# Kernel optimization log

Hardware: AMD Instinct MI355X
Metric: run time of the kernel (lower is better)

Reference implementation:

```python
import jax, jax.numpy as jnp
import numpy as np

DIM = 512
H = 8
HD = DIM // H
B = 1
S = 4096
SCALE = HD ** -0.5


def setup_inputs() -> dict:
    key = jax.random.key(0)
    k1, k2, k3, k4, k5 = jax.random.split(key, 5)
    bound = DIM ** -0.5
    x = jax.random.normal(k1, (B, S, DIM), dtype=jnp.float32)
    q_param = jax.random.uniform(k2, (DIM, H, HD), dtype=jnp.float32, minval=-bound, maxval=bound)
    k_param = jax.random.uniform(k3, (DIM, H, HD), dtype=jnp.float32, minval=-bound, maxval=bound)
    v_param = jax.random.uniform(k4, (DIM, H, HD), dtype=jnp.float32, minval=-bound, maxval=bound)
    p_param = jax.random.uniform(k5, (H, HD, DIM), dtype=jnp.float32, minval=-bound, maxval=bound)
    return {"x": x, "q_param": q_param, "k_param": k_param, "v_param": v_param, "p_param": p_param}


def reference(x, q_param, k_param, v_param, p_param):
    q = jnp.einsum('bsc,chd->bshd', x, q_param) * SCALE
    k = jnp.einsum('btc,chd->bthd', x, k_param)
    v = jnp.einsum('btc,chd->bthd', x, v_param)
    attn = jax.nn.softmax(jnp.einsum('bshd,bthd->bhst', q, k), axis=-1)  # [B,H,S,S]
    o = jnp.einsum('bhst,bthd->bshd', attn, v)
    return jnp.einsum('bshd,hdc->bsc', o, p_param)
```

## Files before the change

### kernel.cpp

```cpp
#include <hip/hip_runtime.h>
#include <hip/hip_bf16.h>
#include <stdint.h>

#define S_LEN 4096
#define DIM   512
#define NH    8
#define HD    64
#define QSCALE 0.18033688011112042f

typedef __attribute__((ext_vector_type(8))) short short8;
typedef __attribute__((ext_vector_type(4))) float f32x4;
typedef __attribute__((ext_vector_type(16))) float f32x16;
typedef __attribute__((ext_vector_type(2))) unsigned uint2v;

__device__ __forceinline__ uint32_t pk2(float lo, float hi) {
  union { __hip_bfloat162 h; uint32_t u; } cv;
  cv.h = __float22bfloat162_rn(float2{lo, hi});
  return cv.u;
}
__device__ __forceinline__ ushort bf1(float x) {
  union { __hip_bfloat16 b; ushort u; } cv;
  cv.b = __float2bfloat16(x);
  return cv.u;
}
__device__ __forceinline__ float bf2f(ushort u) {
  union { uint32_t u; float f; } cv;
  cv.u = (uint32_t)u << 16;
  return cv.f;
}

__global__ __launch_bounds__(256)
void cast_x(const float* __restrict__ src, ushort* __restrict__ dst) {
  const int i = (blockIdx.x * 256 + threadIdx.x) * 8;
  const float4 a = *reinterpret_cast<const float4*>(src + i);
  const float4 b = *reinterpret_cast<const float4*>(src + i + 4);
  uint4 o;
  o.x = pk2(a.x, a.y); o.y = pk2(a.z, a.w);
  o.z = pk2(b.x, b.y); o.w = pk2(b.z, b.w);
  *reinterpret_cast<uint4*>(dst + i) = o;
}

__global__ __launch_bounds__(256)
void transpose_w(const float* __restrict__ qp, const float* __restrict__ kp,
                 const float* __restrict__ vp, const float* __restrict__ pp,
                 ushort* __restrict__ wbT, ushort* __restrict__ ppT) {
  __shared__ float L[64][65];
  const int z = blockIdx.z;
  const float* src = (z == 0) ? qp : (z == 1) ? kp : (z == 2) ? vp : pp;
  ushort* dst = (z < 3) ? (wbT + (size_t)z * 512 * 512) : ppT;
  const float scale = (z == 0) ? QSCALE : 1.0f;
  const int k0 = blockIdx.x * 64, n0 = blockIdx.y * 64;
  const int r = threadIdx.x >> 2, c0 = (threadIdx.x & 3) * 16;

#pragma unroll
  for (int j = 0; j < 4; ++j) {
    const float4 v =
        *reinterpret_cast<const float4*>(&src[(k0 + r) * 512 + n0 + c0 + 4 * j]);
    L[r][c0 + 4 * j + 0] = v.x * scale;
    L[r][c0 + 4 * j + 1] = v.y * scale;
    L[r][c0 + 4 * j + 2] = v.z * scale;
    L[r][c0 + 4 * j + 3] = v.w * scale;
  }
  __syncthreads();

  uint4 u0, u1;
  u0.x = pk2(L[c0 + 0][r], L[c0 + 1][r]);
  u0.y = pk2(L[c0 + 2][r], L[c0 + 3][r]);
  u0.z = pk2(L[c0 + 4][r], L[c0 + 5][r]);
  u0.w = pk2(L[c0 + 6][r], L[c0 + 7][r]);
  u1.x = pk2(L[c0 + 8][r], L[c0 + 9][r]);
  u1.y = pk2(L[c0 + 10][r], L[c0 + 11][r]);
  u1.z = pk2(L[c0 + 12][r], L[c0 + 13][r]);
  u1.w = pk2(L[c0 + 14][r], L[c0 + 15][r]);
  ushort* d = dst + (size_t)(n0 + r) * 512 + k0 + c0;
  *reinterpret_cast<uint4*>(d) = u0;
  *reinterpret_cast<uint4*>(d + 8) = u1;
}

template <int MODE>
__global__ __launch_bounds__(256)
void gemm_bf16(const ushort* __restrict__ A, const ushort* __restrict__ Bt,
               void* __restrict__ Cout) {
  __shared__ __align__(16) unsigned char lds[24576];
  const int tid = threadIdx.x;
  const int m0 = blockIdx.x * 128, n0 = blockIdx.y * 64;
  const int lane = tid & 63, w = tid >> 6;
  const int wm = w >> 1, wn = w & 1;
  const int q = lane & 15, g = lane >> 4;
  f32x4 acc[4][2] = {};

  const int ar = tid >> 1, ah = tid & 1;
  const int br = tid >> 2, bq = tid & 3;

  for (int k0 = 0; k0 < 512; k0 += 64) {
    const ushort* ag = A + (size_t)(m0 + ar) * 512 + k0 + ah * 32;
    const uint4 a0 = *reinterpret_cast<const uint4*>(ag);
    const uint4 a1 = *reinterpret_cast<const uint4*>(ag + 8);
    const uint4 a2 = *reinterpret_cast<const uint4*>(ag + 16);
    const uint4 a3 = *reinterpret_cast<const uint4*>(ag + 24);
    const ushort* bg = Bt + (size_t)(n0 + br) * 512 + k0 + bq * 16;
    const uint4 b0 = *reinterpret_cast<const uint4*>(bg);
    const uint4 b1 = *reinterpret_cast<const uint4*>(bg + 8);
    __syncthreads();
    {
      unsigned char* ab = lds + ar * 128;
      const int asw = (ar & 7) << 4;
      *reinterpret_cast<uint4*>(ab + ((ah * 64 + 0) ^ asw)) = a0;
      *reinterpret_cast<uint4*>(ab + ((ah * 64 + 16) ^ asw)) = a1;
      *reinterpret_cast<uint4*>(ab + ((ah * 64 + 32) ^ asw)) = a2;
      *reinterpret_cast<uint4*>(ab + ((ah * 64 + 48) ^ asw)) = a3;
      unsigned char* bb = lds + 16384 + br * 128;
      const int bsw = (br & 7) << 4;
      *reinterpret_cast<uint4*>(bb + ((bq * 32 + 0) ^ bsw)) = b0;
      *reinterpret_cast<uint4*>(bb + ((bq * 32 + 16) ^ bsw)) = b1;
    }
    __syncthreads();

#pragma unroll
    for (int ks = 0; ks < 2; ++ks) {
      short8 bf[2];
#pragma unroll
      for (int ni = 0; ni < 2; ++ni) {
        const int rn = wn * 32 + ni * 16 + q;
        bf[ni] = *reinterpret_cast<const short8*>(
            lds + 16384 + rn * 128 + ((64 * ks + 16 * g) ^ ((rn & 7) << 4)));
      }
#pragma unroll
      for (int mi = 0; mi < 4; ++mi) {
        const int rm = wm * 64 + mi * 16 + q;
        const short8 af = *reinterpret_cast<const short8*>(
            lds + rm * 128 + ((64 * ks + 16 * g) ^ ((rm & 7) << 4)));
#pragma unroll
        for (int ni = 0; ni < 2; ++ni)
          acc[mi][ni] = __builtin_amdgcn_mfma_f32_16x16x32_bf16(
              af, bf[ni], acc[mi][ni], 0, 0, 0);
      }
    }
  }

  if (MODE == 0) {
    ushort* C = (ushort*)Cout;
    const int which = n0 >> 9;
#pragma unroll
    for (int ni = 0; ni < 2; ++ni) {
      const int n = n0 + wn * 32 + ni * 16 + q;
      const int rem = n & 511, hh = rem >> 6, d = rem & 63;
      if (which == 2) {
        ushort* base = C + (size_t)(2 * NH + hh) * (size_t)(S_LEN * HD) +
                       (size_t)d * S_LEN;
#pragma unroll
        for (int mi = 0; mi < 4; ++mi) {
          const int s = m0 + wm * 64 + mi * 16 + 4 * g;
          uint2 pw;
          pw.x = pk2(acc[mi][ni][0], acc[mi][ni][1]);
          pw.y = pk2(acc[mi][ni][2], acc[mi][ni][3]);
          *reinterpret_cast<uint2*>(base + s) = pw;
        }
      } else {
        ushort* base =
            C + ((size_t)which * NH + hh) * (size_t)(S_LEN * HD) + d;
#pragma unroll
        for (int mi = 0; mi < 4; ++mi) {
          const int s = m0 + wm * 64 + mi * 16 + 4 * g;
#pragma unroll
          for (int r = 0; r < 4; ++r)
            base[(size_t)(s + r) * HD] = bf1(acc[mi][ni][r]);
        }
      }
    }
  } else {
    float* C = (float*)Cout;
#pragma unroll
    for (int ni = 0; ni < 2; ++ni) {
      const int n = n0 + wn * 32 + ni * 16 + q;
#pragma unroll
      for (int mi = 0; mi < 4; ++mi) {
        const int s = m0 + wm * 64 + mi * 16 + 4 * g;
#pragma unroll
        for (int r = 0; r < 4; ++r)
          C[(size_t)(s + r) * 512 + n] = acc[mi][ni][r];
      }
    }
  }
}

__global__ __launch_bounds__(256)
void attn_mfma32(const ushort* __restrict__ QKV, ushort* __restrict__ Opart,
                 float2* __restrict__ ML) {
  __shared__ __align__(16) unsigned char lds[16384];
  const int tid = threadIdx.x;
  const int combo = blockIdx.x;
  const int h = combo & 7, z = combo >> 3;
  const int qb = blockIdx.y;
  const int lane = tid & 63, w = tid >> 6;
  const int r31 = lane & 31, hh = lane >> 5;

  const size_t plane = (size_t)S_LEN * HD;
  const ushort* Qp = QKV + (size_t)h * plane;
  const ushort* Kp = QKV + (size_t)(NH + h) * plane;
  const ushort* Vp = QKV + (size_t)(2 * NH + h) * plane;

  const int qrow = qb * 128 + w * 32 + r31;

  short8 qf[4];
  {
    const ushort* qptr = Qp + (size_t)qrow * HD + 8 * hh;
#pragma unroll
    for (int ks = 0; ks < 4; ++ks)
      qf[ks] = *reinterpret_cast<const short8*>(qptr + 16 * ks);
  }

  int raddr[4];
#pragma unroll
  for (int ks = 0; ks < 4; ++ks)
    raddr[ks] = r31 * 128 + (((2 * ks + hh) ^ (r31 & 7)) << 4);

  const int trow = tid >> 2, seg = tid & 3;
  const int swr = (trow & 7) << 4;
  const int wk0 = trow * 128 + ((seg * 32) ^ swr);
  const int wk1 = trow * 128 + ((seg * 32 + 16) ^ swr);
  const ushort* kgbase = Kp + (size_t)(z * 1024 + trow) * HD + seg * 16;
  const ushort* vgbase = Vp + (size_t)trow * S_LEN + z * 1024 + seg * 16;

  f32x16 o[2] = {};
  float m_i = -1e30f, l_i = 0.f;

  uint4 kA = *reinterpret_cast<const uint4*>(kgbase);
  uint4 kB = *reinterpret_cast<const uint4*>(kgbase + 8);
  uint4 vA = *reinterpret_cast<const uint4*>(vgbase);
  uint4 vB = *reinterpret_cast<const uint4*>(vgbase + 8);

  for (int t = 0; t < 16; ++t) {
    __syncthreads();
    *reinterpret_cast<uint4*>(lds + wk0) = kA;
    *reinterpret_cast<uint4*>(lds + wk1) = kB;
    *reinterpret_cast<uint4*>(lds + 8192 + wk0) = vA;
    *reinterpret_cast<uint4*>(lds + 8192 + wk1) = vB;
    __syncthreads();

    const int tn = (t + 1) & 15;
    kA = *reinterpret_cast<const uint4*>(kgbase + tn * 4096);
    kB = *reinterpret_cast<const uint4*>(kgbase + tn * 4096 + 8);
    vA = *reinterpret_cast<const uint4*>(vgbase + tn * 64);
    vB = *reinterpret_cast<const uint4*>(vgbase + tn * 64 + 8);

    f32x16 s0 = {}, s1 = {};
#pragma unroll
    for (int ks = 0; ks < 4; ++ks) {
      const short8 a0 = *reinterpret_cast<const short8*>(lds + raddr[ks]);
      const short8 a1 = *reinterpret_cast<const short8*>(lds + raddr[ks] + 4096);
      s0 = __builtin_amdgcn_mfma_f32_32x32x16_bf16(a0, qf[ks], s0, 0, 0, 0);
      s1 = __builtin_amdgcn_mfma_f32_32x32x16_bf16(a1, qf[ks], s1, 0, 0, 0);
    }

    float mv[8];
#pragma unroll
    for (int i = 0; i < 8; ++i)
      mv[i] = fmaxf(fmaxf(s0[i], s0[i + 8]), fmaxf(s1[i], s1[i + 8]));
#pragma unroll
    for (int i = 0; i < 4; ++i) mv[i] = fmaxf(mv[i], mv[i + 4]);
    float mx = fmaxf(fmaxf(mv[0], mv[1]), fmaxf(mv[2], mv[3]));
    mx = fmaxf(mx, __shfl_xor(mx, 32));

    const bool grow = mx > m_i + 8.0f;
    if (__any(grow)) {
      const float mn = grow ? mx : m_i;
      const float alpha = grow ? exp2f(m_i - mn) : 1.0f;
      l_i *= alpha;
#pragma unroll
      for (int i = 0; i < 16; ++i) { o[0][i] *= alpha; o[1][i] *= alpha; }
      m_i = mn;
    }

    float r0 = 0.f, r1 = 0.f, r2 = 0.f, r3 = 0.f;
#pragma unroll
    for (int i = 0; i < 16; i += 4) {
      s0[i + 0] = exp2f(s0[i + 0] - m_i); r0 += s0[i + 0];
      s0[i + 1] = exp2f(s0[i + 1] - m_i); r1 += s0[i + 1];
      s0[i + 2] = exp2f(s0[i + 2] - m_i); r2 += s0[i + 2];
      s0[i + 3] = exp2f(s0[i + 3] - m_i); r3 += s0[i + 3];
      s1[i + 0] = exp2f(s1[i + 0] - m_i); r0 += s1[i + 0];
      s1[i + 1] = exp2f(s1[i + 1] - m_i); r1 += s1[i + 1];
      s1[i + 2] = exp2f(s1[i + 2] - m_i); r2 += s1[i + 2];
      s1[i + 3] = exp2f(s1[i + 3] - m_i); r3 += s1[i + 3];
    }
    float rs = (r0 + r1) + (r2 + r3);
    rs += __shfl_xor(rs, 32);
    l_i += rs;

    uint32_t u[2][4][2];
#pragma unroll
    for (int b = 0; b < 4; ++b)
#pragma unroll
      for (int e = 0; e < 2; ++e) {
        u[0][b][e] = pk2(s0[4 * b + 2 * e], s0[4 * b + 2 * e + 1]);
        u[1][b][e] = pk2(s1[4 * b + 2 * e], s1[4 * b + 2 * e + 1]);
      }
    short8 pf[4];
#pragma unroll
    for (int ks = 0; ks < 4; ++ks) {
      const int mt = ks >> 1, bb = 2 * (ks & 1);
      const uint2v se0 =
          __builtin_amdgcn_permlane32_swap(u[mt][bb][0], u[mt][bb + 1][0],
                                           false, false);
      const uint2v se1 =
          __builtin_amdgcn_permlane32_swap(u[mt][bb][1], u[mt][bb + 1][1],
                                           false, false);
      uint32_t fr[4] = {se0.x, se1.x, se0.y, se1.y};
      pf[ks] = *reinterpret_cast<short8*>(fr);
    }

#pragma unroll
    for (int dt = 0; dt < 2; ++dt)
#pragma unroll
      for (int ks = 0; ks < 4; ++ks) {
        const short8 vf = *reinterpret_cast<const short8*>(
            lds + 8192 + dt * 4096 + raddr[ks]);
        o[dt] = __builtin_amdgcn_mfma_f32_32x32x16_bf16(vf, pf[ks], o[dt],
                                                        0, 0, 0);
      }
  }

  if (lane < 32) ML[(size_t)combo * S_LEN + qrow] = float2{m_i, l_i};
  ushort* ob = Opart + (size_t)combo * 64 * S_LEN + qrow;
#pragma unroll
  for (int dt = 0; dt < 2; ++dt)
#pragma unroll
    for (int r = 0; r < 16; ++r) {
      const int d = 32 * dt + (r & 3) + 8 * (r >> 2) + 4 * hh;
      ob[(size_t)d * S_LEN] = bf1(o[dt][r]);
    }
}

__global__ __launch_bounds__(256)
void combine(const ushort* __restrict__ Opart, const float2* __restrict__ ML,
             ushort* __restrict__ ob) {
  const int t = threadIdx.x;
  const int qq = t & 63, ds = t >> 6;
  const int q = blockIdx.x * 64 + qq;
  const int h = blockIdx.y;

  float m = -1e30f, mz[4], lz[4];
#pragma unroll
  for (int z = 0; z < 4; ++z) {
    const float2 v = ML[(size_t)(z * 8 + h) * S_LEN + q];
    mz[z] = v.x; lz[z] = v.y;
    m = fmaxf(m, v.x);
  }
  float wz[4], l = 0.f;
#pragma unroll
  for (int z = 0; z < 4; ++z) {
    wz[z] = exp2f(mz[z] - m);
    l += wz[z] * lz[z];
  }
  const float inv = 1.0f / l;

  float acc[16];
#pragma unroll
  for (int i = 0; i < 16; ++i) acc[i] = 0.f;
#pragma unroll
  for (int z = 0; z < 4; ++z) {
    const ushort* src =
        Opart + ((size_t)(z * 8 + h) * 64 + ds * 16) * S_LEN + q;
#pragma unroll
    for (int i = 0; i < 16; ++i)
      acc[i] += wz[z] * bf2f(src[(size_t)i * S_LEN]);
  }
  uint32_t pk[8];
#pragma unroll
  for (int i = 0; i < 8; ++i)
    pk[i] = pk2(acc[2 * i] * inv, acc[2 * i + 1] * inv);
  ushort* dst = ob + (size_t)q * DIM + h * 64 + ds * 16;
  *reinterpret_cast<uint4*>(dst) = *reinterpret_cast<uint4*>(pk);
  *reinterpret_cast<uint4*>(dst + 8) = *reinterpret_cast<uint4*>(pk + 4);
}

extern "C" void kernel_launch(void* const* d_in, const int* in_sizes, int n_in,
                              void* d_out, int out_size, void* d_ws, size_t ws_size,
                              hipStream_t stream) {
  const float* x  = (const float*)d_in[0];
  const float* qp = (const float*)d_in[1];
  const float* kp = (const float*)d_in[2];
  const float* vp = (const float*)d_in[3];
  const float* pp = (const float*)d_in[4];
  float* out = (float*)d_out;

  unsigned char* ws = (unsigned char*)d_ws;
  ushort* xb    = (ushort*)(ws);
  ushort* qkvb  = (ushort*)(ws + ((size_t)4 << 20));
  ushort* ob    = (ushort*)(ws + ((size_t)16 << 20));
  ushort* wbT   = (ushort*)(ws + ((size_t)20 << 20));
  ushort* ppT   = (ushort*)(ws + ((size_t)22 << 20));
  ushort* opart = (ushort*)(ws + ((size_t)23 << 20));
  float2* ml    = (float2*)(ws + ((size_t)39 << 20));

  cast_x<<<dim3(1024), dim3(256), 0, stream>>>(x, xb);
  transpose_w<<<dim3(8, 8, 4), dim3(256), 0, stream>>>(qp, kp, vp, pp, wbT, ppT);
  gemm_bf16<0><<<dim3(32, 24), dim3(256), 0, stream>>>(xb, wbT, qkvb);
  attn_mfma32<<<dim3(32, 32), dim3(256), 0, stream>>>(qkvb, opart, ml);
  combine<<<dim3(64, 8), dim3(256), 0, stream>>>(opart, ml, ob);
  gemm_bf16<1><<<dim3(32, 8), dim3(256), 0, stream>>>(ob, ppT, out);
}
```

Measured before the change: 112.1 us.

## Double-buffer K/V tiles in LDS and use raw v_exp_f32 in attention

The attention kernel now alternates between two 16KB LDS buffers per iteration. This removes the leading barrier in each loop step, so the next tile's stores can overlap with the current tile's reads. Softmax exponentials switch from exp2f to a raw v_exp_f32 inline asm, dropping the range-handling code that exp2f adds. The P packing is restructured to pack per k-slice, and launch bounds ask for 4 blocks per CU. The costs are doubled LDS per block and loss of denormal/edge handling in exp.

```diff
diff --git a/kernel.cpp b/kernel.cpp
--- a/kernel.cpp
+++ b/kernel.cpp
@@ -27,6 +27,11 @@
   union { uint32_t u; float f; } cv;
   cv.u = (uint32_t)u << 16;
   return cv.f;
+}
+__device__ __forceinline__ float fexp2(float x) {
+  float r;
+  asm("v_exp_f32 %0, %1" : "=v"(r) : "v"(x));
+  return r;
 }
 
 __global__ __launch_bounds__(256)
@@ -184,10 +189,10 @@
   }
 }
 
-__global__ __launch_bounds__(256)
+__global__ __launch_bounds__(256, 4)
 void attn_mfma32(const ushort* __restrict__ QKV, ushort* __restrict__ Opart,
                  float2* __restrict__ ML) {
-  __shared__ __align__(16) unsigned char lds[16384];
+  __shared__ __align__(16) unsigned char lds[32768];
   const int tid = threadIdx.x;
   const int combo = blockIdx.x;
   const int h = combo & 7, z = combo >> 3;
@@ -231,11 +236,11 @@
   uint4 vB = *reinterpret_cast<const uint4*>(vgbase + 8);
 
   for (int t = 0; t < 16; ++t) {
-    __syncthreads();
-    *reinterpret_cast<uint4*>(lds + wk0) = kA;
-    *reinterpret_cast<uint4*>(lds + wk1) = kB;
-    *reinterpret_cast<uint4*>(lds + 8192 + wk0) = vA;
-    *reinterpret_cast<uint4*>(lds + 8192 + wk1) = vB;
+    const int po = (t & 1) << 14;
+    *reinterpret_cast<uint4*>(lds + (wk0 | po)) = kA;
+    *reinterpret_cast<uint4*>(lds + (wk1 | po)) = kB;
+    *reinterpret_cast<uint4*>(lds + ((8192 + wk0) | po)) = vA;
+    *reinterpret_cast<uint4*>(lds + ((8192 + wk1) | po)) = vB;
     __syncthreads();
 
     const int tn = (t + 1) & 15;
@@ -247,8 +252,10 @@
     f32x16 s0 = {}, s1 = {};
 #pragma unroll
     for (int ks = 0; ks < 4; ++ks) {
-      const short8 a0 = *reinterpret_cast<const short8*>(lds + raddr[ks]);
-      const short8 a1 = *reinterpret_cast<const short8*>(lds + raddr[ks] + 4096);
+      const short8 a0 =
+          *reinterpret_cast<const short8*>(lds + (raddr[ks] | po));
+      const short8 a1 =
+          *reinterpret_cast<const short8*>(lds + ((raddr[ks] + 4096) | po));
       s0 = __builtin_amdgcn_mfma_f32_32x32x16_bf16(a0, qf[ks], s0, 0, 0, 0);
       s1 = __builtin_amdgcn_mfma_f32_32x32x16_bf16(a1, qf[ks], s1, 0, 0, 0);
     }
@@ -265,7 +272,7 @@
     const bool grow = mx > m_i + 8.0f;
     if (__any(grow)) {
       const float mn = grow ? mx : m_i;
-      const float alpha = grow ? exp2f(m_i - mn) : 1.0f;
+      const float alpha = grow ? fexp2(m_i - mn) : 1.0f;
       l_i *= alpha;
 #pragma unroll
       for (int i = 0; i < 16; ++i) { o[0][i] *= alpha; o[1][i] *= alpha; }
@@ -275,37 +282,37 @@
     float r0 = 0.f, r1 = 0.f, r2 = 0.f, r3 = 0.f;
 #pragma unroll
     for (int i = 0; i < 16; i += 4) {
-      s0[i + 0] = exp2f(s0[i + 0] - m_i); r0 += s0[i + 0];
-      s0[i + 1] = exp2f(s0[i + 1] - m_i); r1 += s0[i + 1];
-      s0[i + 2] = exp2f(s0[i + 2] - m_i); r2 += s0[i + 2];
-      s0[i + 3] = exp2f(s0[i + 3] - m_i); r3 += s0[i + 3];
-      s1[i + 0] = exp2f(s1[i + 0] - m_i); r0 += s1[i + 0];
-      s1[i + 1] = exp2f(s1[i + 1] - m_i); r1 += s1[i + 1];
-      s1[i + 2] = exp2f(s1[i + 2] - m_i); r2 += s1[i + 2];
-      s1[i + 3] = exp2f(s1[i + 3] - m_i); r3 += s1[i + 3];
+      s0[i + 0] = fexp2(s0[i + 0] - m_i); r0 += s0[i + 0];
+      s0[i + 1] = fexp2(s0[i + 1] - m_i); r1 += s0[i + 1];
+      s0[i + 2] = fexp2(s0[i + 2] - m_i); r2 += s0[i + 2];
+      s0[i + 3] = fexp2(s0[i + 3] - m_i); r3 += s0[i + 3];
+      s1[i + 0] = fexp2(s1[i + 0] - m_i); r0 += s1[i + 0];
+      s1[i + 1] = fexp2(s1[i + 1] - m_i); r1 += s1[i + 1];
+      s1[i + 2] = fexp2(s1[i + 2] - m_i); r2 += s1[i + 2];
+      s1[i + 3] = fexp2(s1[i + 3] - m_i); r3 += s1[i + 3];
     }
     float rs = (r0 + r1) + (r2 + r3);
     rs += __shfl_xor(rs, 32);
     l_i += rs;
 
-    uint32_t u[2][4][2];
-#pragma unroll
-    for (int b = 0; b < 4; ++b)
-#pragma unroll
-      for (int e = 0; e < 2; ++e) {
-        u[0][b][e] = pk2(s0[4 * b + 2 * e], s0[4 * b + 2 * e + 1]);
-        u[1][b][e] = pk2(s1[4 * b + 2 * e], s1[4 * b + 2 * e + 1]);
-      }
     short8 pf[4];
 #pragma unroll
     for (int ks = 0; ks < 4; ++ks) {
-      const int mt = ks >> 1, bb = 2 * (ks & 1);
-      const uint2v se0 =
-          __builtin_amdgcn_permlane32_swap(u[mt][bb][0], u[mt][bb + 1][0],
-                                           false, false);
-      const uint2v se1 =
-          __builtin_amdgcn_permlane32_swap(u[mt][bb][1], u[mt][bb + 1][1],
-                                           false, false);
+      const int bb = 2 * (ks & 1);
+      float p0, p1, p2, p3, p4, p5, p6, p7;
+      if (ks < 2) {
+        p0 = s0[4 * bb + 0]; p1 = s0[4 * bb + 1]; p2 = s0[4 * bb + 2];
+        p3 = s0[4 * bb + 3]; p4 = s0[4 * bb + 4]; p5 = s0[4 * bb + 5];
+        p6 = s0[4 * bb + 6]; p7 = s0[4 * bb + 7];
+      } else {
+        p0 = s1[4 * bb + 0]; p1 = s1[4 * bb + 1]; p2 = s1[4 * bb + 2];
+        p3 = s1[4 * bb + 3]; p4 = s1[4 * bb + 4]; p5 = s1[4 * bb + 5];
+        p6 = s1[4 * bb + 6]; p7 = s1[4 * bb + 7];
+      }
+      const uint32_t u00 = pk2(p0, p1), u01 = pk2(p2, p3);
+      const uint32_t u10 = pk2(p4, p5), u11 = pk2(p6, p7);
+      const uint2v se0 = __builtin_amdgcn_permlane32_swap(u00, u10, false, false);
+      const uint2v se1 = __builtin_amdgcn_permlane32_swap(u01, u11, false, false);
       uint32_t fr[4] = {se0.x, se1.x, se0.y, se1.y};
       pf[ks] = *reinterpret_cast<short8*>(fr);
     }
@@ -315,7 +322,7 @@
 #pragma unroll
       for (int ks = 0; ks < 4; ++ks) {
         const short8 vf = *reinterpret_cast<const short8*>(
-            lds + 8192 + dt * 4096 + raddr[ks]);
+            lds + ((8192 + dt * 4096 + raddr[ks]) | po));
         o[dt] = __builtin_amdgcn_mfma_f32_32x32x16_bf16(vf, pf[ks], o[dt],
                                                         0, 0, 0);
       }
@@ -350,7 +357,7 @@
   float wz[4], l = 0.f;
 #pragma unroll
   for (int z = 0; z < 4; ++z) {
-    wz[z] = exp2f(mz[z] - m);
+    wz[z] = fexp2(mz[z] - m);
     l += wz[z] * lz[z];
   }
   const float inv = 1.0f / l;
```

Result: faster. 96.71 us (-13.7%).

## Double query rows per wave, double-buffer K/V in LDS, row-major partial output

Applied to the files above, without the earlier changes.

Each wave of the attention kernel now handles two 32-row query tiles that share every K/V fragment read from LDS. This halves the K/V LDS reads and the global K/V loads per query, and the grid shrinks to match. K/V staging is double-buffered in LDS so one barrier per iteration replaces two. The l-sum shuffle moves out of the loop, exp2 uses raw v_exp_f32, and the partial outputs are stored row-major with packed vector writes so the combine kernel can read them with 16-byte loads. Costs are higher register pressure and LDS use (launch bounds ask for 2 blocks per SM) and fewer blocks in flight.

```diff
diff --git a/kernel.cpp b/kernel.cpp
--- a/kernel.cpp
+++ b/kernel.cpp
@@ -27,6 +27,11 @@
   union { uint32_t u; float f; } cv;
   cv.u = (uint32_t)u << 16;
   return cv.f;
+}
+__device__ __forceinline__ float fexp2(float x) {
+  float r;
+  asm("v_exp_f32 %0, %1" : "=v"(r) : "v"(x));
+  return r;
 }
 
 __global__ __launch_bounds__(256)
@@ -184,10 +189,10 @@
   }
 }
 
-__global__ __launch_bounds__(256)
+__global__ __launch_bounds__(256, 2)
 void attn_mfma32(const ushort* __restrict__ QKV, ushort* __restrict__ Opart,
                  float2* __restrict__ ML) {
-  __shared__ __align__(16) unsigned char lds[16384];
+  __shared__ __align__(16) unsigned char lds[32768];
   const int tid = threadIdx.x;
   const int combo = blockIdx.x;
   const int h = combo & 7, z = combo >> 3;
@@ -200,135 +205,189 @@
   const ushort* Kp = QKV + (size_t)(NH + h) * plane;
   const ushort* Vp = QKV + (size_t)(2 * NH + h) * plane;
 
-  const int qrow = qb * 128 + w * 32 + r31;
-
-  short8 qf[4];
+  const int qbase = qb * 256 + w * 64;
+  const int qrowA = qbase + r31, qrowB = qbase + 32 + r31;
+
+  short8 qfA[4], qfB[4];
   {
-    const ushort* qptr = Qp + (size_t)qrow * HD + 8 * hh;
-#pragma unroll
-    for (int ks = 0; ks < 4; ++ks)
-      qf[ks] = *reinterpret_cast<const short8*>(qptr + 16 * ks);
-  }
-
-  int raddr[4];
+    const ushort* qa = Qp + (size_t)qrowA * HD + 8 * hh;
+    const ushort* qbp = Qp + (size_t)qrowB * HD + 8 * hh;
+#pragma unroll
+    for (int ks = 0; ks < 4; ++ks) {
+      qfA[ks] = *reinterpret_cast<const short8*>(qa + 16 * ks);
+      qfB[ks] = *reinterpret_cast<const short8*>(qbp + 16 * ks);
+    }
+  }
+
+  int roff[4];
 #pragma unroll
   for (int ks = 0; ks < 4; ++ks)
-    raddr[ks] = r31 * 128 + (((2 * ks + hh) ^ (r31 & 7)) << 4);
+    roff[ks] = (((2 * ks + hh) << 4) ^ ((r31 & 7) << 4));
+  const int rbase = r31 * 128;
 
   const int trow = tid >> 2, seg = tid & 3;
-  const int swr = (trow & 7) << 4;
-  const int wk0 = trow * 128 + ((seg * 32) ^ swr);
-  const int wk1 = trow * 128 + ((seg * 32 + 16) ^ swr);
+  const int tsw = (trow & 7) << 4;
+  const int wk0 = trow * 128 + ((seg * 32) ^ tsw);
+  const int wk1 = trow * 128 + ((seg * 32 + 16) ^ tsw);
   const ushort* kgbase = Kp + (size_t)(z * 1024 + trow) * HD + seg * 16;
   const ushort* vgbase = Vp + (size_t)trow * S_LEN + z * 1024 + seg * 16;
 
-  f32x16 o[2] = {};
-  float m_i = -1e30f, l_i = 0.f;
-
-  uint4 kA = *reinterpret_cast<const uint4*>(kgbase);
-  uint4 kB = *reinterpret_cast<const uint4*>(kgbase + 8);
-  uint4 vA = *reinterpret_cast<const uint4*>(vgbase);
-  uint4 vB = *reinterpret_cast<const uint4*>(vgbase + 8);
+  f32x16 oA[2] = {}, oB[2] = {};
+  float mA = -1e30f, lA = 0.f, mB = -1e30f, lB = 0.f;
+
+  uint4 kst0 = *reinterpret_cast<const uint4*>(kgbase);
+  uint4 kst1 = *reinterpret_cast<const uint4*>(kgbase + 8);
+  uint4 vst0 = *reinterpret_cast<const uint4*>(vgbase);
+  uint4 vst1 = *reinterpret_cast<const uint4*>(vgbase + 8);
 
   for (int t = 0; t < 16; ++t) {
+    const int po = (t & 1) << 14;
+    *reinterpret_cast<uint4*>(lds + (wk0 | po)) = kst0;
+    *reinterpret_cast<uint4*>(lds + (wk1 | po)) = kst1;
+    *reinterpret_cast<uint4*>(lds + ((8192 + wk0) | po)) = vst0;
+    *reinterpret_cast<uint4*>(lds + ((8192 + wk1) | po)) = vst1;
     __syncthreads();
-    *reinterpret_cast<uint4*>(lds + wk0) = kA;
-    *reinterpret_cast<uint4*>(lds + wk1) = kB;
-    *reinterpret_cast<uint4*>(lds + 8192 + wk0) = vA;
-    *reinterpret_cast<uint4*>(lds + 8192 + wk1) = vB;
-    __syncthreads();
 
     const int tn = (t + 1) & 15;
-    kA = *reinterpret_cast<const uint4*>(kgbase + tn * 4096);
-    kB = *reinterpret_cast<const uint4*>(kgbase + tn * 4096 + 8);
-    vA = *reinterpret_cast<const uint4*>(vgbase + tn * 64);
-    vB = *reinterpret_cast<const uint4*>(vgbase + tn * 64 + 8);
-
-    f32x16 s0 = {}, s1 = {};
-#pragma unroll
-    for (int ks = 0; ks < 4; ++ks) {
-      const short8 a0 = *reinterpret_cast<const short8*>(lds + raddr[ks]);
-      const short8 a1 = *reinterpret_cast<const short8*>(lds + raddr[ks] + 4096);
-      s0 = __builtin_amdgcn_mfma_f32_32x32x16_bf16(a0, qf[ks], s0, 0, 0, 0);
-      s1 = __builtin_amdgcn_mfma_f32_32x32x16_bf16(a1, qf[ks], s1, 0, 0, 0);
-    }
-
-    float mv[8];
-#pragma unroll
-    for (int i = 0; i < 8; ++i)
-      mv[i] = fmaxf(fmaxf(s0[i], s0[i + 8]), fmaxf(s1[i], s1[i + 8]));
-#pragma unroll
-    for (int i = 0; i < 4; ++i) mv[i] = fmaxf(mv[i], mv[i + 4]);
-    float mx = fmaxf(fmaxf(mv[0], mv[1]), fmaxf(mv[2], mv[3]));
-    mx = fmaxf(mx, __shfl_xor(mx, 32));
-
-    const bool grow = mx > m_i + 8.0f;
-    if (__any(grow)) {
-      const float mn = grow ? mx : m_i;
-      const float alpha = grow ? exp2f(m_i - mn) : 1.0f;
-      l_i *= alpha;
-#pragma unroll
-      for (int i = 0; i < 16; ++i) { o[0][i] *= alpha; o[1][i] *= alpha; }
-      m_i = mn;
-    }
-
-    float r0 = 0.f, r1 = 0.f, r2 = 0.f, r3 = 0.f;
-#pragma unroll
-    for (int i = 0; i < 16; i += 4) {
-      s0[i + 0] = exp2f(s0[i + 0] - m_i); r0 += s0[i + 0];
-      s0[i + 1] = exp2f(s0[i + 1] - m_i); r1 += s0[i + 1];
-      s0[i + 2] = exp2f(s0[i + 2] - m_i); r2 += s0[i + 2];
-      s0[i + 3] = exp2f(s0[i + 3] - m_i); r3 += s0[i + 3];
-      s1[i + 0] = exp2f(s1[i + 0] - m_i); r0 += s1[i + 0];
-      s1[i + 1] = exp2f(s1[i + 1] - m_i); r1 += s1[i + 1];
-      s1[i + 2] = exp2f(s1[i + 2] - m_i); r2 += s1[i + 2];
-      s1[i + 3] = exp2f(s1[i + 3] - m_i); r3 += s1[i + 3];
-    }
-    float rs = (r0 + r1) + (r2 + r3);
-    rs += __shfl_xor(rs, 32);
-    l_i += rs;
-
-    uint32_t u[2][4][2];
-#pragma unroll
-    for (int b = 0; b < 4; ++b)
+    kst0 = *reinterpret_cast<const uint4*>(kgbase + tn * 4096);
+    kst1 = *reinterpret_cast<const uint4*>(kgbase + tn * 4096 + 8);
+    vst0 = *reinterpret_cast<const uint4*>(vgbase + tn * 64);
+    vst1 = *reinterpret_cast<const uint4*>(vgbase + tn * 64 + 8);
+
+#pragma unroll
+    for (int c = 0; c < 2; ++c) {
+      f32x16 sA = {}, sB = {};
+#pragma unroll
+      for (int ks = 0; ks < 4; ++ks) {
+        const short8 af = *reinterpret_cast<const short8*>(
+            lds + ((c * 4096 + rbase + roff[ks]) | po));
+        sA = __builtin_amdgcn_mfma_f32_32x32x16_bf16(af, qfA[ks], sA, 0, 0, 0);
+        sB = __builtin_amdgcn_mfma_f32_32x32x16_bf16(af, qfB[ks], sB, 0, 0, 0);
+      }
+
+      {
+        float mv[8];
+#pragma unroll
+        for (int i = 0; i < 8; ++i) mv[i] = fmaxf(sA[i], sA[i + 8]);
+#pragma unroll
+        for (int i = 0; i < 4; ++i) mv[i] = fmaxf(mv[i], mv[i + 4]);
+        float mx = fmaxf(fmaxf(mv[0], mv[1]), fmaxf(mv[2], mv[3]));
+        mx = fmaxf(mx, __shfl_xor(mx, 32));
+        const bool grow = mx > mA + 8.0f;
+        if (__any(grow)) {
+          const float mn = grow ? mx : mA;
+          const float alpha = grow ? fexp2(mA - mn) : 1.0f;
+          lA *= alpha;
+#pragma unroll
+          for (int i = 0; i < 16; ++i) { oA[0][i] *= alpha; oA[1][i] *= alpha; }
+          mA = mn;
+        }
+        float r0 = 0.f, r1 = 0.f, r2 = 0.f, r3 = 0.f;
+#pragma unroll
+        for (int i = 0; i < 16; i += 4) {
+          sA[i + 0] = fexp2(sA[i + 0] - mA); r0 += sA[i + 0];
+          sA[i + 1] = fexp2(sA[i + 1] - mA); r1 += sA[i + 1];
+          sA[i + 2] = fexp2(sA[i + 2] - mA); r2 += sA[i + 2];
+          sA[i + 3] = fexp2(sA[i + 3] - mA); r3 += sA[i + 3];
+        }
+        lA += (r0 + r1) + (r2 + r3);
+      }
+      {
+        float mv[8];
+#pragma unroll
+        for (int i = 0; i < 8; ++i) mv[i] = fmaxf(sB[i], sB[i + 8]);
+#pragma unroll
+        for (int i = 0; i < 4; ++i) mv[i] = fmaxf(mv[i], mv[i + 4]);
+        float mx = fmaxf(fmaxf(mv[0], mv[1]), fmaxf(mv[2], mv[3]));
+        mx = fmaxf(mx, __shfl_xor(mx, 32));
+        const bool grow = mx > mB + 8.0f;
+        if (__any(grow)) {
+          const float mn = grow ? mx : mB;
+          const float alpha = grow ? fexp2(mB - mn) : 1.0f;
+          lB *= alpha;
+#pragma unroll
+          for (int i = 0; i < 16; ++i) { oB[0][i] *= alpha; oB[1][i] *= alpha; }
+          mB = mn;
+        }
+        float r0 = 0.f, r1 = 0.f, r2 = 0.f, r3 = 0.f;
+#pragma unroll
+        for (int i = 0; i < 16; i += 4) {
+          sB[i + 0] = fexp2(sB[i + 0] - mB); r0 += sB[i + 0];
+          sB[i + 1] = fexp2(sB[i + 1] - mB); r1 += sB[i + 1];
+          sB[i + 2] = fexp2(sB[i + 2] - mB); r2 += sB[i + 2];
+          sB[i + 3] = fexp2(sB[i + 3] - mB); r3 += sB[i + 3];
+        }
+        lB += (r0 + r1) + (r2 + r3);
+      }
+
+      short8 pfA[2], pfB[2];
 #pragma unroll
       for (int e = 0; e < 2; ++e) {
-        u[0][b][e] = pk2(s0[4 * b + 2 * e], s0[4 * b + 2 * e + 1]);
-        u[1][b][e] = pk2(s1[4 * b + 2 * e], s1[4 * b + 2 * e + 1]);
-      }
-    short8 pf[4];
-#pragma unroll
-    for (int ks = 0; ks < 4; ++ks) {
-      const int mt = ks >> 1, bb = 2 * (ks & 1);
-      const uint2v se0 =
-          __builtin_amdgcn_permlane32_swap(u[mt][bb][0], u[mt][bb + 1][0],
-                                           false, false);
-      const uint2v se1 =
-          __builtin_amdgcn_permlane32_swap(u[mt][bb][1], u[mt][bb + 1][1],
-                                           false, false);
-      uint32_t fr[4] = {se0.x, se1.x, se0.y, se1.y};
-      pf[ks] = *reinterpret_cast<short8*>(fr);
-    }
-
-#pragma unroll
-    for (int dt = 0; dt < 2; ++dt)
-#pragma unroll
-      for (int ks = 0; ks < 4; ++ks) {
-        const short8 vf = *reinterpret_cast<const short8*>(
-            lds + 8192 + dt * 4096 + raddr[ks]);
-        o[dt] = __builtin_amdgcn_mfma_f32_32x32x16_bf16(vf, pf[ks], o[dt],
-                                                        0, 0, 0);
-      }
-  }
-
-  if (lane < 32) ML[(size_t)combo * S_LEN + qrow] = float2{m_i, l_i};
-  ushort* ob = Opart + (size_t)combo * 64 * S_LEN + qrow;
+        const int bb = 2 * e;
+        {
+          const uint32_t u00 = pk2(sA[4 * bb + 0], sA[4 * bb + 1]);
+          const uint32_t u01 = pk2(sA[4 * bb + 2], sA[4 * bb + 3]);
+          const uint32_t u10 = pk2(sA[4 * bb + 4], sA[4 * bb + 5]);
+          const uint32_t u11 = pk2(sA[4 * bb + 6], sA[4 * bb + 7]);
+          const uint2v se0 =
+              __builtin_amdgcn_permlane32_swap(u00, u10, false, false);
+          const uint2v se1 =
+              __builtin_amdgcn_permlane32_swap(u01, u11, false, false);
+          uint32_t fr[4] = {se0.x, se1.x, se0.y, se1.y};
+          pfA[e] = *reinterpret_cast<short8*>(fr);
+        }
+        {
+          const uint32_t u00 = pk2(sB[4 * bb + 0], sB[4 * bb + 1]);
+          const uint32_t u01 = pk2(sB[4 * bb + 2], sB[4 * bb + 3]);
+          const uint32_t u10 = pk2(sB[4 * bb + 4], sB[4 * bb + 5]);
+          const uint32_t u11 = pk2(sB[4 * bb + 6], sB[4 * bb + 7]);
+          const uint2v se0 =
+              __builtin_amdgcn_permlane32_swap(u00, u10, false, false);
+          const uint2v se1 =
+              __builtin_amdgcn_permlane32_swap(u01, u11, false, false);
+          uint32_t fr[4] = {se0.x, se1.x, se0.y, se1.y};
+          pfB[e] = *reinterpret_cast<short8*>(fr);
+        }
+      }
+
+#pragma unroll
+      for (int dt = 0; dt < 2; ++dt)
+#pragma unroll
+        for (int e = 0; e < 2; ++e) {
+          const int kg = 2 * c + e;
+          const short8 vf = *reinterpret_cast<const short8*>(
+              lds + ((8192 + (32 * dt + r31) * 128 +
+                      (((32 * kg + 16 * hh)) ^ ((r31 & 7) << 4))) |
+                     po));
+          oA[dt] = __builtin_amdgcn_mfma_f32_32x32x16_bf16(vf, pfA[e], oA[dt],
+                                                           0, 0, 0);
+          oB[dt] = __builtin_amdgcn_mfma_f32_32x32x16_bf16(vf, pfB[e], oB[dt],
+                                                           0, 0, 0);
+        }
+    }
+  }
+
+  lA += __shfl_xor(lA, 32);
+  lB += __shfl_xor(lB, 32);
+
+  if (lane < 32) {
+    ML[(size_t)combo * S_LEN + qrowA] = float2{mA, lA};
+    ML[(size_t)combo * S_LEN + qrowB] = float2{mB, lB};
+  }
+  ushort* obA = Opart + ((size_t)combo * S_LEN + qrowA) * HD;
+  ushort* obB = Opart + ((size_t)combo * S_LEN + qrowB) * HD;
 #pragma unroll
   for (int dt = 0; dt < 2; ++dt)
 #pragma unroll
-    for (int r = 0; r < 16; ++r) {
-      const int d = 32 * dt + (r & 3) + 8 * (r >> 2) + 4 * hh;
-      ob[(size_t)d * S_LEN] = bf1(o[dt][r]);
+    for (int rq = 0; rq < 4; ++rq) {
+      const int d = 32 * dt + 8 * rq + 4 * hh;
+      uint2 pwA, pwB;
+      pwA.x = pk2(oA[dt][4 * rq + 0], oA[dt][4 * rq + 1]);
+      pwA.y = pk2(oA[dt][4 * rq + 2], oA[dt][4 * rq + 3]);
+      pwB.x = pk2(oB[dt][4 * rq + 0], oB[dt][4 * rq + 1]);
+      pwB.y = pk2(oB[dt][4 * rq + 2], oB[dt][4 * rq + 3]);
+      *reinterpret_cast<uint2*>(obA + d) = pwA;
+      *reinterpret_cast<uint2*>(obB + d) = pwB;
     }
 }
 
@@ -350,10 +409,12 @@
   float wz[4], l = 0.f;
 #pragma unroll
   for (int z = 0; z < 4; ++z) {
-    wz[z] = exp2f(mz[z] - m);
+    wz[z] = fexp2(mz[z] - m);
     l += wz[z] * lz[z];
   }
   const float inv = 1.0f / l;
+#pragma unroll
+  for (int z = 0; z < 4; ++z) wz[z] *= inv;
 
   float acc[16];
 #pragma unroll
@@ -361,15 +422,21 @@
 #pragma unroll
   for (int z = 0; z < 4; ++z) {
     const ushort* src =
-        Opart + ((size_t)(z * 8 + h) * 64 + ds * 16) * S_LEN + q;
-#pragma unroll
-    for (int i = 0; i < 16; ++i)
-      acc[i] += wz[z] * bf2f(src[(size_t)i * S_LEN]);
+        Opart + (((size_t)(z * 8 + h) * S_LEN) + q) * HD + ds * 16;
+    const uint4 u0 = *reinterpret_cast<const uint4*>(src);
+    const uint4 u1 = *reinterpret_cast<const uint4*>(src + 8);
+    const ushort* e0 = reinterpret_cast<const ushort*>(&u0);
+    const ushort* e1 = reinterpret_cast<const ushort*>(&u1);
+#pragma unroll
+    for (int i = 0; i < 8; ++i) {
+      acc[i] = fmaf(wz[z], bf2f(e0[i]), acc[i]);
+      acc[i + 8] = fmaf(wz[z], bf2f(e1[i]), acc[i + 8]);
+    }
   }
   uint32_t pk[8];
 #pragma unroll
   for (int i = 0; i < 8; ++i)
-    pk[i] = pk2(acc[2 * i] * inv, acc[2 * i + 1] * inv);
+    pk[i] = pk2(acc[2 * i], acc[2 * i + 1]);
   ushort* dst = ob + (size_t)q * DIM + h * 64 + ds * 16;
   *reinterpret_cast<uint4*>(dst) = *reinterpret_cast<uint4*>(pk);
   *reinterpret_cast<uint4*>(dst + 8) = *reinterpret_cast<uint4*>(pk + 4);
@@ -397,7 +464,7 @@
   cast_x<<<dim3(1024), dim3(256), 0, stream>>>(x, xb);
   transpose_w<<<dim3(8, 8, 4), dim3(256), 0, stream>>>(qp, kp, vp, pp, wbT, ppT);
   gemm_bf16<0><<<dim3(32, 24), dim3(256), 0, stream>>>(xb, wbT, qkvb);
-  attn_mfma32<<<dim3(32, 32), dim3(256), 0, stream>>>(qkvb, opart, ml);
+  attn_mfma32<<<dim3(32, 16), dim3(256), 0, stream>>>(qkvb, opart, ml);
   combine<<<dim3(64, 8), dim3(256), 0, stream>>>(opart, ml, ob);
   gemm_bf16<1><<<dim3(32, 8), dim3(256), 0, stream>>>(ob, ppT, out);
 }
```

Result: faster. 94.30 us (-15.8%).
